# Optimization experiments

Hardware: AMD Instinct MI355X
Metric: run time of the kernel (lower is better)

The kernel has to match this reference:

```python
import jax, jax.numpy as jnp
import numpy as np

EPS = 1e-8
L_TEMEL, L_DENGE, L_CPU, L_SURU, L_NASH = 1.0, 0.1, 0.05, 0.03, 0.02


def setup_inputs() -> dict:
    key = jax.random.key(0)
    ks = jax.random.split(key, 8)
    N_tok, V = 8192, 32000
    N_birim, D, K = 100000, 64, 16
    return {
        "tahminler": jax.random.normal(ks[0], (N_tok, V), dtype=jnp.float32),
        "hedefler": jax.random.randint(ks[1], (N_tok,), 0, V),
        "is_yuku_dagilimi": jax.random.uniform(ks[2], (N_birim,), dtype=jnp.float32),
        "onbellek_durumu": jax.random.uniform(ks[3], (N_birim,), dtype=jnp.float32),
        "secilen_indeksler": jax.random.randint(ks[4], (N_tok,), 0, N_birim),
        "birim_stratejileri": jax.random.normal(ks[5], (N_birim, D), dtype=jnp.float32),
        "komsu_indeksleri": jax.random.randint(ks[6], (N_birim, K), 0, N_birim),
        "oyuncu_kazanimlari": jax.random.uniform(ks[7], (N_birim,), dtype=jnp.float32),
        "mevcut_stratejiler": jax.random.normal(jax.random.fold_in(key, 99), (N_birim, D), dtype=jnp.float32),
    }


def _var_mean_ratio(x):
    # torch.var is unbiased (ddof=1)
    return jnp.var(x, ddof=1) / (jnp.mean(x) + EPS)


def _suru_uyum(strat, komsu_idx):
    # strat: [N, D], komsu_idx: [N, K]
    komsu = strat[komsu_idx]                 # [N, K, D] ragged-gather (uniform degree)
    ort_komsu = jnp.mean(komsu, axis=1)      # [N, D]
    bn = jnp.linalg.norm(strat, axis=-1)     # [N]
    kn = jnp.linalg.norm(ort_komsu, axis=-1) # [N]
    dots = jnp.einsum("nd,nd->n", strat, ort_komsu)
    valid = (bn > EPS) & (kn > EPS)
    cos = jnp.where(valid, dots / jnp.where(valid, bn * kn, 1.0), 0.0)
    cnt = jnp.sum(valid)
    uyum = jnp.where(cnt > 0, jnp.sum(cos) / jnp.maximum(cnt, 1), 0.0)
    return (uyum + 1.0) / 2.0


def reference(tahminler, hedefler, is_yuku_dagilimi, onbellek_durumu,
              secilen_indeksler, birim_stratejileri, komsu_indeksleri,
              oyuncu_kazanimlari, mevcut_stratejiler):
    # 1) CrossEntropyLoss (mean over tokens)
    logp = jax.nn.log_softmax(tahminler, axis=-1)
    temel = -jnp.take_along_axis(logp, hedefler[:, None], axis=1).mean()
    # 2) workload balance: var/mean
    dengeleme = _var_mean_ratio(is_yuku_dagilimi)
    # 3) cache hit-rate on selected indices
    cpu = jnp.mean(onbellek_durumu[secilen_indeksler])
    # 4) swarm cohesion via neighbor cosine similarity
    suru = _suru_uyum(birim_stratejileri, komsu_indeksleri)
    # 5) Nash regularization: var/mean of payoffs (mevcut_stratejiler unused, as in torch)
    nash = _var_mean_ratio(oyuncu_kazanimlari)
    toplam = (L_TEMEL * temel + L_DENGE * dengeleme - L_CPU * cpu
              - L_SURU * suru + L_NASH * nash)
    return jnp.stack([toplam, temel, dengeleme, cpu, suru, nash])
```

## Files before the change

### kernel.cpp

```cpp
#include <hip/hip_runtime.h>
#include <hip/hip_bf16.h>

#define WS_CE 0
#define WS_YSUM 1
#define WS_YSQ 2
#define WS_GATHER 3
#define WS_COS 4
#define WS_CNT 5
#define WS_OSUM 6
#define WS_OSQ 7

#define SURU_BLOCKS 256
#define STAT_BLOCKS 64
#define GATHER_BLOCKS 32
#define PRE_BLOCKS (SURU_BLOCKS + 2 * STAT_BLOCKS + GATHER_BLOCKS)

typedef float f32x4 __attribute__((ext_vector_type(4)));

__device__ __forceinline__ float wave_sum(float v) {
#pragma unroll
    for (int off = 32; off > 0; off >>= 1) v += __shfl_xor(v, off, 64);
    return v;
}

__global__ void init_ws_kernel(float* ws) {
    if (threadIdx.x < 8) ws[threadIdx.x] = 0.f;
}

__global__ __launch_bounds__(256, 4) void fused_kernel(
    const float* __restrict__ logits, const int* __restrict__ targets, int V, int n_tok,
    const float* __restrict__ yuku, const float* __restrict__ oyun, int n_birim,
    const float* __restrict__ onbellek, const int* __restrict__ secilen,
    const float* __restrict__ strat, const int* __restrict__ komsu, int K,
    float* ws) {
    __shared__ float sh_a[4], sh_b[4];
    const int b = blockIdx.x;
    const int wid = threadIdx.x >> 6;
    const int lane = threadIdx.x & 63;

    if (b >= PRE_BLOCKS) {
        const int row = b - PRE_BLOCKS;
        const float* rowp = logits + (size_t)row * V;
        const f32x4* rp = (const f32x4*)rowp;
        const int nvec = V >> 2;
        float s0 = 0.f, s1 = 0.f, s2 = 0.f, s3 = 0.f;
        int i = threadIdx.x;
        for (; i + 768 < nvec; i += 1024) {
            f32x4 a = __builtin_nontemporal_load(rp + i);
            f32x4 c = __builtin_nontemporal_load(rp + i + 256);
            f32x4 d = __builtin_nontemporal_load(rp + i + 512);
            f32x4 e = __builtin_nontemporal_load(rp + i + 768);
            s0 += __expf(a.x); s1 += __expf(a.y); s2 += __expf(a.z); s3 += __expf(a.w);
            s0 += __expf(c.x); s1 += __expf(c.y); s2 += __expf(c.z); s3 += __expf(c.w);
            s0 += __expf(d.x); s1 += __expf(d.y); s2 += __expf(d.z); s3 += __expf(d.w);
            s0 += __expf(e.x); s1 += __expf(e.y); s2 += __expf(e.z); s3 += __expf(e.w);
        }
        for (; i < nvec; i += 256) {
            f32x4 v = __builtin_nontemporal_load(rp + i);
            s0 += __expf(v.x); s1 += __expf(v.y); s2 += __expf(v.z); s3 += __expf(v.w);
        }
        float s = (s0 + s1) + (s2 + s3);
        s = wave_sum(s);
        if (lane == 0) sh_a[wid] = s;
        __syncthreads();
        if (threadIdx.x == 0) {
            float S = sh_a[0] + sh_a[1] + sh_a[2] + sh_a[3];
            float xt = rowp[targets[row]];
            atomicAdd(ws + WS_CE, logf(S) - xt);
        }
        return;
    }

    if (b < SURU_BLOCKS) {
        const int nwave = SURU_BLOCKS * 4;
        float cos_sum = 0.f, cnt = 0.f;
        if (K == 16) {
            for (int u = b * 4 + wid; u < n_birim; u += nwave) {
                float own = strat[(size_t)u * 64 + lane];
                const int* kp = komsu + (size_t)u * 16;
                int idx[16];
#pragma unroll
                for (int k = 0; k < 16; ++k) idx[k] = kp[k];
                float g[16];
#pragma unroll
                for (int k = 0; k < 16; ++k) g[k] = strat[(size_t)idx[k] * 64 + lane];
                float acc = 0.f;
#pragma unroll
                for (int k = 0; k < 16; ++k) acc += g[k];
                float ort = acc * (1.f / 16.f);
                float dot = wave_sum(own * ort);
                float b2 = wave_sum(own * own);
                float k2 = wave_sum(ort * ort);
                float bn = sqrtf(b2), knrm = sqrtf(k2);
                if (bn > 1e-8f && knrm > 1e-8f) {
                    cos_sum += dot / (bn * knrm);
                    cnt += 1.f;
                }
            }
        } else {
            for (int u = b * 4 + wid; u < n_birim; u += nwave) {
                float own = strat[(size_t)u * 64 + lane];
                const int* kp = komsu + (size_t)u * K;
                float acc = 0.f;
                for (int k = 0; k < K; ++k)
                    acc += strat[(size_t)kp[k] * 64 + lane];
                float ort = acc / (float)K;
                float dot = wave_sum(own * ort);
                float b2 = wave_sum(own * own);
                float k2 = wave_sum(ort * ort);
                float bn = sqrtf(b2), knrm = sqrtf(k2);
                if (bn > 1e-8f && knrm > 1e-8f) {
                    cos_sum += dot / (bn * knrm);
                    cnt += 1.f;
                }
            }
        }
        if (lane == 0) { sh_a[wid] = cos_sum; sh_b[wid] = cnt; }
        __syncthreads();
        if (threadIdx.x == 0) {
            atomicAdd(ws + WS_COS, sh_a[0] + sh_a[1] + sh_a[2] + sh_a[3]);
            atomicAdd(ws + WS_CNT, sh_b[0] + sh_b[1] + sh_b[2] + sh_b[3]);
        }
        return;
    }

    if (b < SURU_BLOCKS + 2 * STAT_BLOCKS) {
        const int sb = b - SURU_BLOCKS;
        const bool is_oyun = sb >= STAT_BLOCKS;
        const int sbb = is_oyun ? sb - STAT_BLOCKS : sb;
        const float* x = is_oyun ? oyun : yuku;
        const int sum_idx = is_oyun ? WS_OSUM : WS_YSUM;
        const int sq_idx = is_oyun ? WS_OSQ : WS_YSQ;
        float s = 0.f, sq = 0.f;
        for (int i = sbb * 256 + threadIdx.x; i < n_birim; i += STAT_BLOCKS * 256) {
            float v = x[i];
            s += v;
            sq += v * v;
        }
        s = wave_sum(s);
        sq = wave_sum(sq);
        if (lane == 0) { sh_a[wid] = s; sh_b[wid] = sq; }
        __syncthreads();
        if (threadIdx.x == 0) {
            atomicAdd(ws + sum_idx, sh_a[0] + sh_a[1] + sh_a[2] + sh_a[3]);
            atomicAdd(ws + sq_idx, sh_b[0] + sh_b[1] + sh_b[2] + sh_b[3]);
        }
        return;
    }

    {
        const int gb = b - SURU_BLOCKS - 2 * STAT_BLOCKS;
        float s = 0.f;
        for (int i = gb * 256 + threadIdx.x; i < n_tok; i += GATHER_BLOCKS * 256)
            s += onbellek[secilen[i]];
        s = wave_sum(s);
        if (lane == 0) sh_a[wid] = s;
        __syncthreads();
        if (threadIdx.x == 0)
            atomicAdd(ws + WS_GATHER, sh_a[0] + sh_a[1] + sh_a[2] + sh_a[3]);
    }
}

__global__ void finalize_kernel(const float* __restrict__ ws, float* __restrict__ out,
                                int n_tok, int n_birim) {
    if (threadIdx.x != 0 || blockIdx.x != 0) return;
    const float n = (float)n_birim;
    float temel = ws[WS_CE] / (float)n_tok;

    float ysum = ws[WS_YSUM];
    float ymean = ysum / n;
    float yvar = (ws[WS_YSQ] - ysum * ysum / n) / (n - 1.f);
    float denge = yvar / (ymean + 1e-8f);

    float cpu = ws[WS_GATHER] / (float)n_tok;

    float cnt = ws[WS_CNT];
    float uyum = cnt > 0.f ? ws[WS_COS] / fmaxf(cnt, 1.f) : 0.f;
    float suru = (uyum + 1.f) * 0.5f;

    float osum = ws[WS_OSUM];
    float omean = osum / n;
    float ovar = (ws[WS_OSQ] - osum * osum / n) / (n - 1.f);
    float nash = ovar / (omean + 1e-8f);

    float toplam = 1.0f * temel + 0.1f * denge - 0.05f * cpu - 0.03f * suru + 0.02f * nash;
    out[0] = toplam;
    out[1] = temel;
    out[2] = denge;
    out[3] = cpu;
    out[4] = suru;
    out[5] = nash;
}

extern "C" void kernel_launch(void* const* d_in, const int* in_sizes, int n_in,
                              void* d_out, int out_size, void* d_ws, size_t ws_size,
                              hipStream_t stream) {
    const float* tahminler = (const float*)d_in[0];
    const int* hedefler = (const int*)d_in[1];
    const float* yuku = (const float*)d_in[2];
    const float* onbellek = (const float*)d_in[3];
    const int* secilen = (const int*)d_in[4];
    const float* strat = (const float*)d_in[5];
    const int* komsu = (const int*)d_in[6];
    const float* oyun = (const float*)d_in[7];

    const int n_tok = in_sizes[1];
    const int V = in_sizes[0] / n_tok;
    const int n_birim = in_sizes[2];
    const int K = in_sizes[6] / n_birim;

    float* ws = (float*)d_ws;
    float* out = (float*)d_out;

    init_ws_kernel<<<1, 64, 0, stream>>>(ws);
    fused_kernel<<<PRE_BLOCKS + n_tok, 256, 0, stream>>>(
        tahminler, hedefler, V, n_tok,
        yuku, oyun, n_birim,
        onbellek, secilen,
        strat, komsu, K, ws);
    finalize_kernel<<<1, 64, 0, stream>>>(ws, out, n_tok, n_birim);
}
```

Before: 259.3 us.

## Use persistent CE blocks looping over rows and raise occupancy target

The cross-entropy part now launches a fixed grid of 2048 blocks that each loop over several rows, keeping a local sum and issuing one atomic per block rather than one per row. The row loads use a wave-contiguous layout and plain loads instead of nontemporal loads. Launch bounds rise to 8 blocks per CU, and the neighbor gather is split into two halves of 8 to reduce register pressure. This aims to cut block scheduling and atomic overhead and raise occupancy, but adds extra barriers per row and may lose the streaming hint on the large logits read.

```diff
diff --git a/kernel.cpp b/kernel.cpp
--- a/kernel.cpp
+++ b/kernel.cpp
@@ -14,6 +14,7 @@
 #define STAT_BLOCKS 64
 #define GATHER_BLOCKS 32
 #define PRE_BLOCKS (SURU_BLOCKS + 2 * STAT_BLOCKS + GATHER_BLOCKS)
+#define CE_BLOCKS 2048
 
 typedef float f32x4 __attribute__((ext_vector_type(4)));
 
@@ -27,7 +28,7 @@
     if (threadIdx.x < 8) ws[threadIdx.x] = 0.f;
 }
 
-__global__ __launch_bounds__(256, 4) void fused_kernel(
+__global__ __launch_bounds__(256, 8) void fused_kernel(
     const float* __restrict__ logits, const int* __restrict__ targets, int V, int n_tok,
     const float* __restrict__ yuku, const float* __restrict__ oyun, int n_birim,
     const float* __restrict__ onbellek, const int* __restrict__ secilen,
@@ -39,35 +40,42 @@
     const int lane = threadIdx.x & 63;
 
     if (b >= PRE_BLOCKS) {
-        const int row = b - PRE_BLOCKS;
-        const float* rowp = logits + (size_t)row * V;
-        const f32x4* rp = (const f32x4*)rowp;
         const int nvec = V >> 2;
-        float s0 = 0.f, s1 = 0.f, s2 = 0.f, s3 = 0.f;
-        int i = threadIdx.x;
-        for (; i + 768 < nvec; i += 1024) {
-            f32x4 a = __builtin_nontemporal_load(rp + i);
-            f32x4 c = __builtin_nontemporal_load(rp + i + 256);
-            f32x4 d = __builtin_nontemporal_load(rp + i + 512);
-            f32x4 e = __builtin_nontemporal_load(rp + i + 768);
-            s0 += __expf(a.x); s1 += __expf(a.y); s2 += __expf(a.z); s3 += __expf(a.w);
-            s0 += __expf(c.x); s1 += __expf(c.y); s2 += __expf(c.z); s3 += __expf(c.w);
-            s0 += __expf(d.x); s1 += __expf(d.y); s2 += __expf(d.z); s3 += __expf(d.w);
-            s0 += __expf(e.x); s1 += __expf(e.y); s2 += __expf(e.z); s3 += __expf(e.w);
-        }
-        for (; i < nvec; i += 256) {
-            f32x4 v = __builtin_nontemporal_load(rp + i);
-            s0 += __expf(v.x); s1 += __expf(v.y); s2 += __expf(v.z); s3 += __expf(v.w);
-        }
-        float s = (s0 + s1) + (s2 + s3);
-        s = wave_sum(s);
-        if (lane == 0) sh_a[wid] = s;
-        __syncthreads();
-        if (threadIdx.x == 0) {
-            float S = sh_a[0] + sh_a[1] + sh_a[2] + sh_a[3];
-            float xt = rowp[targets[row]];
-            atomicAdd(ws + WS_CE, logf(S) - xt);
-        }
+        const int nmain = nvec & ~1023;
+        const int base = wid * 256 + lane;
+        float ce_local = 0.f;
+        for (int row = b - PRE_BLOCKS; row < n_tok; row += CE_BLOCKS) {
+            const float* rowp = logits + (size_t)row * V;
+            const f32x4* rp = (const f32x4*)rowp;
+            float s0 = 0.f, s1 = 0.f, s2 = 0.f, s3 = 0.f;
+            for (int t = 0; t < nmain; t += 1024) {
+                const f32x4* p = rp + t + base;
+                f32x4 v0 = p[0];
+                f32x4 v1 = p[64];
+                f32x4 v2 = p[128];
+                f32x4 v3 = p[192];
+                s0 += __expf(v0.x); s1 += __expf(v0.y); s2 += __expf(v0.z); s3 += __expf(v0.w);
+                s0 += __expf(v1.x); s1 += __expf(v1.y); s2 += __expf(v1.z); s3 += __expf(v1.w);
+                s0 += __expf(v2.x); s1 += __expf(v2.y); s2 += __expf(v2.z); s3 += __expf(v2.w);
+                s0 += __expf(v3.x); s1 += __expf(v3.y); s2 += __expf(v3.z); s3 += __expf(v3.w);
+            }
+            for (int v = nmain + (int)threadIdx.x; v < nvec; v += 256) {
+                f32x4 x = rp[v];
+                s0 += __expf(x.x); s1 += __expf(x.y); s2 += __expf(x.z); s3 += __expf(x.w);
+            }
+            float s = (s0 + s1) + (s2 + s3);
+            s = wave_sum(s);
+            if (lane == 0) sh_a[wid] = s;
+            __syncthreads();
+            if (threadIdx.x == 0) {
+                float S = sh_a[0] + sh_a[1] + sh_a[2] + sh_a[3];
+                float xt = rowp[targets[row]];
+                ce_local += logf(S) - xt;
+            }
+            __syncthreads();
+        }
+        if (threadIdx.x == 0 && ce_local != 0.f)
+            atomicAdd(ws + WS_CE, ce_local);
         return;
     }
 
@@ -78,15 +86,18 @@
             for (int u = b * 4 + wid; u < n_birim; u += nwave) {
                 float own = strat[(size_t)u * 64 + lane];
                 const int* kp = komsu + (size_t)u * 16;
-                int idx[16];
-#pragma unroll
-                for (int k = 0; k < 16; ++k) idx[k] = kp[k];
-                float g[16];
-#pragma unroll
-                for (int k = 0; k < 16; ++k) g[k] = strat[(size_t)idx[k] * 64 + lane];
                 float acc = 0.f;
 #pragma unroll
-                for (int k = 0; k < 16; ++k) acc += g[k];
+                for (int h = 0; h < 2; ++h) {
+                    int idx[8];
+#pragma unroll
+                    for (int k = 0; k < 8; ++k) idx[k] = kp[h * 8 + k];
+                    float g[8];
+#pragma unroll
+                    for (int k = 0; k < 8; ++k) g[k] = strat[(size_t)idx[k] * 64 + lane];
+#pragma unroll
+                    for (int k = 0; k < 8; ++k) acc += g[k];
+                }
                 float ort = acc * (1.f / 16.f);
                 float dot = wave_sum(own * ort);
                 float b2 = wave_sum(own * own);
@@ -213,7 +224,7 @@
     float* out = (float*)d_out;
 
     init_ws_kernel<<<1, 64, 0, stream>>>(ws);
-    fused_kernel<<<PRE_BLOCKS + n_tok, 256, 0, stream>>>(
+    fused_kernel<<<PRE_BLOCKS + CE_BLOCKS, 256, 0, stream>>>(
         tahminler, hedefler, V, n_tok,
         yuku, oyun, n_birim,
         onbellek, secilen,
```

Result: slower. 269.2 us (+3.8%).
